# Kernel optimization log

Measured on AMD Instinct MI355X. Metric: run time of the kernel, lower is better.

Reference implementation:

```python
import jax, jax.numpy as jnp
import numpy as np

B, S, H = 2, 2048, 2048
NH, G = 16, 4
HD = H // NH          # 128
REP = NH // G         # 4 query heads per KV group
KV = G * HD           # 512


def setup_inputs() -> dict:
    key = jax.random.key(0)
    ks = jax.random.split(key, 10)
    s = 0.02
    X = jax.random.normal(ks[0], (B, S, H), dtype=jnp.float32)
    Wq = jax.random.normal(ks[1], (H, H), dtype=jnp.float32) * s
    bq = jnp.zeros((H,), dtype=jnp.float32)
    Wk = jax.random.normal(ks[2], (H, KV), dtype=jnp.float32) * s
    bk = jnp.zeros((KV,), dtype=jnp.float32)
    Wv = jax.random.normal(ks[3], (H, KV), dtype=jnp.float32) * s
    bv = jnp.zeros((KV,), dtype=jnp.float32)
    Wo = jax.random.normal(ks[4], (H, H), dtype=jnp.float32) * s
    bo = jnp.zeros((H,), dtype=jnp.float32)
    # causal mask: 1 where attention is disallowed (strict upper triangle)
    casual_mask = jnp.triu(jnp.ones((S, S), dtype=jnp.float32), k=1)[None, None]
    return {"X": X, "Wq": Wq, "bq": bq, "Wk": Wk, "bk": bk,
            "Wv": Wv, "bv": bv, "Wo": Wo, "bo": bo,
            "casual_mask": casual_mask}


def reference(X, Wq, bq, Wk, bk, Wv, bv, Wo, bo, casual_mask):
    # projections
    q = X @ Wq + bq                          # [B,S,H]
    k = X @ Wk + bk                          # [B,S,G*HD]
    v = X @ Wv + bv                          # [B,S,G*HD]
    # split heads; q grouped as (group, rep) to match torch expand ordering
    q = q.reshape(B, S, NH, HD).transpose(0, 2, 1, 3)       # [B,NH,S,HD]
    q = q.reshape(B, G, REP, S, HD)                          # [B,G,REP,S,HD]
    k = k.reshape(B, S, G, HD).transpose(0, 2, 1, 3)         # [B,G,S,HD]
    v = v.reshape(B, S, G, HD).transpose(0, 2, 1, 3)         # [B,G,S,HD]
    scale = 1.0 / jnp.sqrt(jnp.float32(HD))
    scores = jnp.einsum('bgrqd,bgkd->bgrqk', q, k) * scale   # [B,G,REP,S,S]
    scores = scores + casual_mask * (-1e9)
    probs = jax.nn.softmax(scores, axis=-1)
    out = jnp.einsum('bgrqk,bgkd->bgrqd', probs, v)          # [B,G,REP,S,HD]
    out = out.reshape(B, NH, S, HD).transpose(0, 2, 1, 3).reshape(B, S, H)
    return out @ Wo + bo
```

## Files before the change

kernel.cpp:

```cpp
#include <hip/hip_runtime.h>

#define B_   2
#define S_   2048
#define H_   2048
#define NH_  16
#define G_   4
#define HD_  128
#define KV_  512
#define HQKV 3072

typedef __attribute__((ext_vector_type(8))) short bf16x8;
typedef __attribute__((ext_vector_type(4))) float f32x4;

__device__ __forceinline__ unsigned short f2bf(float f) {
    unsigned u = __float_as_uint(f);
    u += 0x7fff + ((u >> 16) & 1);
    return (unsigned short)(u >> 16);
}
__device__ __forceinline__ float bf2f(unsigned short s) {
    return __uint_as_float(((unsigned)s) << 16);
}
__device__ __forceinline__ unsigned cvtpk(float a, float b) {
    unsigned r;
    asm volatile("v_cvt_pk_bf16_f32 %0, %1, %2" : "=v"(r) : "v"(a), "v"(b));
    return r;
}

#define GLDS16(gsrc, ldst)                                                            \
    __builtin_amdgcn_global_load_lds(                                                 \
        (const __attribute__((address_space(1))) void*)(gsrc),                        \
        (__attribute__((address_space(3))) void*)(ldst), 16, 0, 0)

#define SC2F (0.08838834764831843f * 1.4426950408889634f)

__global__ void k_cvt_bf16(const float* __restrict__ in, unsigned short* __restrict__ out, int n4) {
    int i = blockIdx.x * blockDim.x + threadIdx.x;
    if (i >= n4) return;
    float4 v = ((const float4*)in)[i];
    ushort4 o;
    o.x = f2bf(v.x); o.y = f2bf(v.y); o.z = f2bf(v.z); o.w = f2bf(v.w);
    ((ushort4*)out)[i] = o;
}

__global__ void k_transpose_cvt(const float* __restrict__ in, unsigned short* __restrict__ out,
                                int R, int C) {
    __shared__ float t[32][33];
    int c0 = blockIdx.x * 32, r0 = blockIdx.y * 32;
    int tx = threadIdx.x, ty = threadIdx.y;
#pragma unroll
    for (int i = 0; i < 4; ++i)
        t[ty + i*8][tx] = in[(size_t)(r0 + ty + i*8) * C + c0 + tx];
    __syncthreads();
#pragma unroll
    for (int i = 0; i < 4; ++i)
        out[(size_t)(c0 + ty + i*8) * R + r0 + tx] = f2bf(t[tx][ty + i*8]);
}

__global__ void k_transpose_qkv(const float* __restrict__ Wq, const float* __restrict__ Wk,
                                const float* __restrict__ Wv, unsigned short* __restrict__ out) {
    __shared__ float t[32][33];
    int n0g = blockIdx.x * 32;
    int h0 = blockIdx.y * 32;
    const float* src; int C, n0l;
    if (n0g < H_)            { src = Wq; C = H_;  n0l = n0g; }
    else if (n0g < H_ + KV_) { src = Wk; C = KV_; n0l = n0g - H_; }
    else                     { src = Wv; C = KV_; n0l = n0g - H_ - KV_; }
    int tx = threadIdx.x, ty = threadIdx.y;
#pragma unroll
    for (int i = 0; i < 4; ++i)
        t[ty + i*8][tx] = src[(size_t)(h0 + ty + i*8) * C + n0l + tx];
    __syncthreads();
#pragma unroll
    for (int i = 0; i < 4; ++i)
        out[(size_t)(n0g + ty + i*8) * H_ + h0 + tx] = f2bf(t[tx][ty + i*8]);
}

__global__ void k_concat_bias(const float* __restrict__ bq, const float* __restrict__ bk,
                              const float* __restrict__ bv, float* __restrict__ out) {
    int i = blockIdx.x * 256 + threadIdx.x;
    if (i >= HQKV) return;
    out[i] = (i < H_) ? bq[i] : (i < H_ + KV_ ? bk[i - H_] : bv[i - H_ - KV_]);
}

__global__ void k_transpose_v(const unsigned short* __restrict__ in, unsigned short* __restrict__ out) {
    __shared__ unsigned short t[32][33];
    int b = blockIdx.z;
    int c0 = blockIdx.x * 32, s0 = blockIdx.y * 32;
    int tx = threadIdx.x, ty = threadIdx.y;
#pragma unroll
    for (int i = 0; i < 4; ++i)
        t[ty + i*8][tx] = in[((size_t)b * S_ + s0 + ty + i*8) * HQKV + (H_ + KV_) + c0 + tx];
    __syncthreads();
#pragma unroll
    for (int i = 0; i < 4; ++i)
        out[((size_t)b * KV_ + c0 + ty + i*8) * S_ + s0 + tx] = t[tx][ty + i*8];
}

template <bool BF16OUT, bool QSCALE>
__global__ __launch_bounds__(512, 2) void k_gemm256(
    const unsigned short* __restrict__ A, const unsigned short* __restrict__ Bt,
    const float* __restrict__ bias, void* __restrict__ Cout, int M, int N, int K) {
    __shared__ __align__(16) unsigned short As[2][256 * 64];
    __shared__ __align__(16) unsigned short Bs[2][256 * 64];
    const int tid = threadIdx.x, lane = tid & 63;
    const int w = tid >> 6;
    const int l15 = lane & 15, l4 = lane >> 4;
    const int wr = w >> 2, wc = w & 3;
    const int m0 = blockIdx.x * 256, n0 = blockIdx.y * 256;
    f32x4 acc[8][4] = {};

    auto stageA = [&](int buf, int kt, int h) {
#pragma unroll
        for (int i = 0; i < 2; ++i) {
            int p = i * 512 + tid;
            int j = p >> 3;
            int row = h * 64 + (j >> 6) * 128 + (j & 63);
            int sc = p & 7;
            int c = sc ^ (row & 7);
            GLDS16(A + (size_t)(m0 + row) * K + kt * 64 + c * 8,
                   &As[buf][(row * 8 + sc) * 8]);
        }
    };
    auto stageB = [&](int buf, int kt, int h) {
#pragma unroll
        for (int i = 0; i < 2; ++i) {
            int p = i * 512 + tid;
            int j = p >> 3;
            int row = h * 32 + (j >> 5) * 64 + (j & 31);
            int sc = p & 7;
            int c = sc ^ (row & 7);
            GLDS16(Bt + (size_t)(n0 + row) * K + kt * 64 + c * 8,
                   &Bs[buf][(row * 8 + sc) * 8]);
        }
    };

    const int NT = K >> 6;
    stageB(0, 0, 0); stageA(0, 0, 0); stageB(0, 0, 1); stageA(0, 0, 1);
    stageB(1, 1, 0); stageA(1, 1, 0);

    bf16x8 bf[2][2];
    for (int t = 0; t < NT; ++t) {
        const int cur = t & 1, nxt = cur ^ 1;
        if (t == NT - 1) { asm volatile("s_waitcnt vmcnt(0)" ::: "memory"); }
        else             { asm volatile("s_waitcnt vmcnt(4)" ::: "memory"); }
        __builtin_amdgcn_s_barrier();
        __builtin_amdgcn_sched_barrier(0);

#pragma unroll
        for (int q = 0; q < 4; ++q) {
            const int nh = q >> 1, mh = q & 1;
            bf16x8 af[4][2];
#pragma unroll
            for (int mf2 = 0; mf2 < 4; ++mf2)
#pragma unroll
                for (int ks = 0; ks < 2; ++ks) {
                    int row = wr * 128 + (mh * 4 + mf2) * 16 + l15;
                    int ch = (ks * 4 + l4) ^ (row & 7);
                    af[mf2][ks] = *(const bf16x8*)(&As[cur][(row * 8 + ch) * 8]);
                }
            if (mh == 0) {
#pragma unroll
                for (int nf2 = 0; nf2 < 2; ++nf2)
#pragma unroll
                    for (int ks = 0; ks < 2; ++ks) {
                        int row = wc * 64 + (nh * 2 + nf2) * 16 + l15;
                        int ch = (ks * 4 + l4) ^ (row & 7);
                        bf[nf2][ks] = *(const bf16x8*)(&Bs[cur][(row * 8 + ch) * 8]);
                    }
            }
            if (q == 0)      { if (t + 1 < NT) stageB(nxt, t + 1, 1); }
            else if (q == 1) { if (t + 1 < NT) stageA(nxt, t + 1, 1); }
            else if (q == 2) { if (t + 2 < NT) stageB(cur, t + 2, 0); }
            else             { if (t + 2 < NT) stageA(cur, t + 2, 0); }

            __builtin_amdgcn_sched_barrier(0);
            __builtin_amdgcn_s_barrier();
            asm volatile("s_waitcnt lgkmcnt(0)" ::: "memory");
            __builtin_amdgcn_sched_barrier(0);
            __builtin_amdgcn_s_setprio(1);
#pragma unroll
            for (int mf2 = 0; mf2 < 4; ++mf2)
#pragma unroll
                for (int nf2 = 0; nf2 < 2; ++nf2)
#pragma unroll
                    for (int ks = 0; ks < 2; ++ks)
                        acc[mh * 4 + mf2][nh * 2 + nf2] = __builtin_amdgcn_mfma_f32_16x16x32_bf16(
                            af[mf2][ks], bf[nf2][ks], acc[mh * 4 + mf2][nh * 2 + nf2], 0, 0, 0);
            __builtin_amdgcn_s_setprio(0);
            __builtin_amdgcn_s_barrier();
        }
    }

#pragma unroll
    for (int mf = 0; mf < 8; ++mf) {
        int row = m0 + wr * 128 + mf * 16 + l4 * 4;
#pragma unroll
        for (int nf = 0; nf < 4; ++nf) {
            int col = n0 + wc * 64 + nf * 16 + l15;
            float bv = bias[col];
#pragma unroll
            for (int r = 0; r < 4; ++r) {
                float v = acc[mf][nf][r] + bv;
                if (QSCALE) { if (col < H_) v *= SC2F; }
                if (BF16OUT)
                    ((unsigned short*)Cout)[(size_t)(row + r) * N + col] = f2bf(v);
                else
                    ((float*)Cout)[(size_t)(row + r) * N + col] = v;
            }
        }
    }
}

template <bool BF16OUT, bool QSCALE>
__global__ __launch_bounds__(256) void k_gemm_bt(
    const unsigned short* __restrict__ A, const unsigned short* __restrict__ Bt,
    const float* __restrict__ bias, void* __restrict__ Cout, int M, int N, int K) {
    __shared__ __align__(16) unsigned short As[128 * 64];
    __shared__ __align__(16) unsigned short Bs[128 * 64];
    const int tid = threadIdx.x, lane = tid & 63, w = tid >> 6;
    const int l15 = lane & 15, l4 = lane >> 4;
    const int wr = w >> 1, wc = w & 1;
    const int m0 = blockIdx.x * 128, n0 = blockIdx.y * 128;
    f32x4 acc[4][4] = {};

    for (int kt = 0; kt < K; kt += 64) {
        __syncthreads();
#pragma unroll
        for (int i = 0; i < 4; ++i) {
            int p = (w * 4 + i) * 64 + lane;
            int row = p >> 3, c = (p & 7) ^ (row & 7);
            GLDS16(A + (size_t)(m0 + row) * K + kt + c * 8, As + (size_t)(w * 4 + i) * 512);
        }
#pragma unroll
        for (int i = 0; i < 4; ++i) {
            int p = (w * 4 + i) * 64 + lane;
            int row = p >> 3, c = (p & 7) ^ (row & 7);
            GLDS16(Bt + (size_t)(n0 + row) * K + kt + c * 8, Bs + (size_t)(w * 4 + i) * 512);
        }
        __syncthreads();
#pragma unroll
        for (int ks = 0; ks < 2; ++ks) {
            bf16x8 af[4], bfr[4];
#pragma unroll
            for (int m = 0; m < 4; ++m) {
                int row = wr * 64 + m * 16 + l15;
                int ch = (ks * 4 + l4) ^ (row & 7);
                af[m] = *(const bf16x8*)(As + row * 64 + ch * 8);
            }
#pragma unroll
            for (int n = 0; n < 4; ++n) {
                int row = wc * 64 + n * 16 + l15;
                int ch = (ks * 4 + l4) ^ (row & 7);
                bfr[n] = *(const bf16x8*)(Bs + row * 64 + ch * 8);
            }
#pragma unroll
            for (int m = 0; m < 4; ++m)
#pragma unroll
                for (int n = 0; n < 4; ++n)
                    acc[m][n] = __builtin_amdgcn_mfma_f32_16x16x32_bf16(af[m], bfr[n], acc[m][n], 0, 0, 0);
        }
    }
#pragma unroll
    for (int m = 0; m < 4; ++m) {
        int row = m0 + wr * 64 + m * 16 + l4 * 4;
#pragma unroll
        for (int n = 0; n < 4; ++n) {
            int col = n0 + wc * 64 + n * 16 + l15;
            float bv = bias[col];
#pragma unroll
            for (int r = 0; r < 4; ++r) {
                float v = acc[m][n][r] + bv;
                if (QSCALE) { if (col < H_) v *= SC2F; }
                if (BF16OUT)
                    ((unsigned short*)Cout)[(size_t)(row + r) * N + col] = f2bf(v);
                else
                    ((float*)Cout)[(size_t)(row + r) * N + col] = v;
            }
        }
    }
}

__global__ __launch_bounds__(256, 4) void k_flash(
    const unsigned short* __restrict__ QKV,
    const unsigned short* __restrict__ VT,
    unsigned short* __restrict__ Oa,
    unsigned short* __restrict__ part1,
    float* __restrict__ mlbuf) {
    __shared__ __align__(16) unsigned short Ks[64 * 128];
    __shared__ __align__(16) unsigned short Vs[128 * 64];
    const int tid = threadIdx.x, lane = tid & 63, w = tid >> 6;
    const int l15 = lane & 15, l4 = lane >> 4;
    const int bid = blockIdx.x;
    const int xcd = bid & 7, idx = bid >> 3;
    const int bh = xcd * 4 + (idx & 3);
    const int jidx = idx >> 2;
    const int b = bh >> 4, nh = bh & 15, g = nh >> 2;

    int qt, t0, t1, mode;
    if (jidx < 16) { qt = 16 + jidx; t0 = 0; t1 = 16; mode = 1; }
    else {
        int k = jidx - 16, j = k >> 1;
        if ((k & 1) == 0) { qt = 31 - j; t0 = 16; t1 = qt + 1; mode = 2; }
        else              { qt = 15 - j; t0 = 0;  t1 = qt + 1; mode = 0; }
    }
    const int qbase = qt * 64 + w * 16;

    const unsigned short* kgbase = QKV + (size_t)b * S_ * HQKV + H_ + g * HD_;
    const unsigned short* vgbase = VT + ((size_t)b * KV_ + g * HD_) * S_;

    auto issueK = [&](int kt) {
        const int kv0 = kt * 64;
#pragma unroll
        for (int i = 0; i < 4; ++i) {
            int p = i * 256 + tid;
            int row = p >> 4, c = (p & 15) ^ (row & 15);
            GLDS16(kgbase + (size_t)(kv0 + row) * HQKV + c * 8, &Ks[(i * 256 + w * 64) * 8]);
        }
    };
    auto issueV = [&](int kt) {
        const int kv0 = kt * 64;
#pragma unroll
        for (int i = 0; i < 4; ++i) {
            int p = i * 256 + tid;
            int row = p >> 3, c = (p & 7) ^ (row & 7);
            GLDS16(vgbase + (size_t)row * S_ + kv0 + c * 8, &Vs[(i * 256 + w * 64) * 8]);
        }
    };

    bf16x8 qf[4];
#pragma unroll
    for (int kb = 0; kb < 4; ++kb)
        qf[kb] = *(const bf16x8*)(QKV + (size_t)(b * S_ + qbase + l15) * HQKV +
                                  nh * HD_ + kb * 32 + l4 * 8);

    f32x4 o[8] = {};
    float m_r = -1e30f, l_r = 0.f;

    const int src0 = l15 + 16 * ((2 * l4) & 3);
    const int src1 = l15 + 16 * ((2 * l4 + 1) & 3);
    const bool hsel = ((l4 >> 1) & 1) != 0;

    issueK(t0);
    issueV(t0);

    for (int kt = t0; kt < t1; ++kt) {
        const int kv0 = kt * 64;
        asm volatile("s_waitcnt vmcnt(4)" ::: "memory");
        __builtin_amdgcn_s_barrier();
        __builtin_amdgcn_sched_barrier(0);

        f32x4 s[4] = {};
#pragma unroll
        for (int kb = 0; kb < 4; ++kb) {
            bf16x8 kf[4];
#pragma unroll
            for (int n = 0; n < 4; ++n) {
                int row = n * 16 + l15;
                int sl = (kb * 4 + l4) ^ (row & 15);
                kf[n] = *(const bf16x8*)(&Ks[(row * 16 + sl) * 8]);
            }
            __builtin_amdgcn_s_setprio(1);
#pragma unroll
            for (int n = 0; n < 4; ++n)
                s[n] = __builtin_amdgcn_mfma_f32_16x16x32_bf16(kf[n], qf[kb], s[n], 0, 0, 0);
            __builtin_amdgcn_s_setprio(0);
        }
        if (kv0 + 63 > qbase) {
            const int qrow = qbase + l15;
#pragma unroll
            for (int n = 0; n < 4; ++n)
#pragma unroll
                for (int r = 0; r < 4; ++r) {
                    int kcol = kv0 + n * 16 + l4 * 4 + r;
                    if (kcol > qrow) s[n][r] = -1e30f;
                }
        }
        float pmax = s[0][0];
#pragma unroll
        for (int n = 0; n < 4; ++n)
#pragma unroll
            for (int r = 0; r < 4; ++r) pmax = fmaxf(pmax, s[n][r]);
        pmax = fmaxf(pmax, __shfl_xor(pmax, 16));
        pmax = fmaxf(pmax, __shfl_xor(pmax, 32));
        if (__any(pmax > m_r + 8.0f)) {
            float mn = fmaxf(m_r, pmax);
            float sf = exp2f(m_r - mn);
            m_r = mn;
            l_r *= sf;
#pragma unroll
            for (int nc = 0; nc < 8; ++nc) {
                f32x4 t = o[nc];
                t[0] *= sf; t[1] *= sf; t[2] *= sf; t[3] *= sf;
                o[nc] = t;
            }
        }
        float rsum = 0.f;
#pragma unroll
        for (int n = 0; n < 4; ++n)
#pragma unroll
            for (int r = 0; r < 4; ++r) {
                float p = exp2f(s[n][r] - m_r);
                s[n][r] = p;
                rsum += p;
            }
        rsum += __shfl_xor(rsum, 16);
        rsum += __shfl_xor(rsum, 32);
        l_r += rsum;

        unsigned plo[4], phi[4];
#pragma unroll
        for (int n = 0; n < 4; ++n) {
            plo[n] = cvtpk(s[n][0], s[n][1]);
            phi[n] = cvtpk(s[n][2], s[n][3]);
        }

        asm volatile("s_waitcnt vmcnt(0)" ::: "memory");
        __builtin_amdgcn_s_barrier();
        __builtin_amdgcn_sched_barrier(0);
        if (kt + 1 < t1) issueK(kt + 1);

#pragma unroll
        for (int kb = 0; kb < 2; ++kb) {
            const int n0i = 2 * kb, n1i = 2 * kb + 1;
            unsigned a0, a1, w0, w1, w2, w3;
            a0 = __shfl((int)plo[n0i], src0); a1 = __shfl((int)plo[n1i], src0); w0 = hsel ? a1 : a0;
            a0 = __shfl((int)phi[n0i], src0); a1 = __shfl((int)phi[n1i], src0); w1 = hsel ? a1 : a0;
            a0 = __shfl((int)plo[n0i], src1); a1 = __shfl((int)plo[n1i], src1); w2 = hsel ? a1 : a0;
            a0 = __shfl((int)phi[n0i], src1); a1 = __shfl((int)phi[n1i], src1); w3 = hsel ? a1 : a0;
            int4 pw = make_int4((int)w0, (int)w1, (int)w2, (int)w3);
            bf16x8 pf = *(bf16x8*)&pw;
            __builtin_amdgcn_s_setprio(1);
#pragma unroll
            for (int nc = 0; nc < 8; ++nc) {
                int row = nc * 16 + l15;
                int sl = (kb * 4 + l4) ^ (row & 7);
                bf16x8 vf = *(const bf16x8*)(&Vs[(row * 8 + sl) * 8]);
                o[nc] = __builtin_amdgcn_mfma_f32_16x16x32_bf16(vf, pf, o[nc], 0, 0, 0);
            }
            __builtin_amdgcn_s_setprio(0);
        }

        __builtin_amdgcn_s_barrier();
        __builtin_amdgcn_sched_barrier(0);
        if (kt + 1 < t1) issueV(kt + 1);
    }

    const int qrow = qbase + l15;
    if (mode == 0) {
        float inv = 1.0f / l_r;
        size_t base = (size_t)(b * S_ + qrow) * H_ + nh * HD_ + l4 * 4;
#pragma unroll
        for (int nc = 0; nc < 8; ++nc) {
            uint2 pk;
            pk.x = cvtpk(o[nc][0] * inv, o[nc][1] * inv);
            pk.y = cvtpk(o[nc][2] * inv, o[nc][3] * inv);
            *(uint2*)(Oa + base + nc * 16) = pk;
        }
    } else {
        const int base = bh * 16 + (qt - 16);
        const int c = (mode == 1) ? 0 : 1;
        float* mlrec = mlbuf + (size_t)(base * 2 + c) * 64 * 2;
        if (l4 == 0) {
            int row = w * 16 + l15;
            mlrec[row * 2 + 0] = m_r;
            mlrec[row * 2 + 1] = l_r;
        }
        if (mode == 1) {
            size_t ob = (size_t)(b * S_ + qrow) * H_ + nh * HD_ + l4 * 4;
#pragma unroll
            for (int nc = 0; nc < 8; ++nc) {
                uint2 pk;
                pk.x = cvtpk(o[nc][0], o[nc][1]);
                pk.y = cvtpk(o[nc][2], o[nc][3]);
                *(uint2*)(Oa + ob + nc * 16) = pk;
            }
        } else {
            size_t pb = ((size_t)base * 64 + w * 16 + l15) * 128 + l4 * 4;
#pragma unroll
            for (int nc = 0; nc < 8; ++nc) {
                uint2 pk;
                pk.x = cvtpk(o[nc][0], o[nc][1]);
                pk.y = cvtpk(o[nc][2], o[nc][3]);
                *(uint2*)(part1 + pb + nc * 16) = pk;
            }
        }
    }
}

__global__ __launch_bounds__(256) void k_combine(
    const float* __restrict__ mlbuf, const unsigned short* __restrict__ part1,
    unsigned short* __restrict__ Oa) {
    int rec = blockIdx.x;
    int bh = rec >> 4, qt = 16 + (rec & 15);
    int b = bh >> 4, nh = bh & 15;
    int row = threadIdx.x >> 2;
    int dseg = (threadIdx.x & 3) * 32;
    const float* ml0 = mlbuf + (size_t)(rec * 2 + 0) * 128;
    const float* ml1 = mlbuf + (size_t)(rec * 2 + 1) * 128;
    float m0 = ml0[row * 2], l0 = ml0[row * 2 + 1];
    float m1 = ml1[row * 2], l1 = ml1[row * 2 + 1];
    float M = fmaxf(m0, m1);
    float a0 = exp2f(m0 - M), a1 = exp2f(m1 - M);
    float L = a0 * l0 + a1 * l1;
    float s0 = a0 / L, s1 = a1 / L;
    size_t ob = ((size_t)(b * S_) + qt * 64 + row) * H_ + nh * HD_ + dseg;
    const unsigned short* p1 = part1 + ((size_t)rec * 64 + row) * 128 + dseg;
#pragma unroll
    for (int i = 0; i < 4; ++i) {
        bf16x8 v0 = *(const bf16x8*)(Oa + ob + i * 8);
        bf16x8 v1 = *(const bf16x8*)(p1 + i * 8);
        bf16x8 oo;
#pragma unroll
        for (int e = 0; e < 8; ++e)
            oo[e] = (short)f2bf(bf2f((unsigned short)v0[e]) * s0 +
                                bf2f((unsigned short)v1[e]) * s1);
        *(bf16x8*)(Oa + ob + i * 8) = oo;
    }
}

extern "C" void kernel_launch(void* const* d_in, const int* in_sizes, int n_in,
                              void* d_out, int out_size, void* d_ws, size_t ws_size,
                              hipStream_t stream) {
    const float* X  = (const float*)d_in[0];
    const float* Wq = (const float*)d_in[1];
    const float* bq = (const float*)d_in[2];
    const float* Wk = (const float*)d_in[3];
    const float* bk = (const float*)d_in[4];
    const float* Wv = (const float*)d_in[5];
    const float* bv = (const float*)d_in[6];
    const float* Wo = (const float*)d_in[7];
    const float* bo = (const float*)d_in[8];
    float* out = (float*)d_out;

    if (ws_size < 80000000) return;
    char* ws = (char*)d_ws;
    unsigned short* Xb    = (unsigned short*)(ws);
    unsigned short* WqkvT = (unsigned short*)(ws + 16777216);
    unsigned short* WoT   = (unsigned short*)(ws + 29360128);
    unsigned short* QKV   = (unsigned short*)(ws + 37748736);
    unsigned short* VbT   = (unsigned short*)(ws + 62914560);
    unsigned short* part1 = (unsigned short*)(ws + 67108864);
    float*          mlbuf = (float*)(ws + 75497472);
    float*          bqkv  = (float*)(ws + 76021760);
    unsigned short* AOb   = Xb;

    k_cvt_bf16<<<(B_ * S_ * H_ / 4 + 255) / 256, 256, 0, stream>>>(X, Xb, B_ * S_ * H_ / 4);
    k_transpose_qkv<<<dim3(HQKV / 32, H_ / 32), dim3(32, 8), 0, stream>>>(Wq, Wk, Wv, WqkvT);
    k_transpose_cvt<<<dim3(H_ / 32, H_ / 32), dim3(32, 8), 0, stream>>>(Wo, WoT, H_, H_);
    k_concat_bias<<<(HQKV + 255) / 256, 256, 0, stream>>>(bq, bk, bv, bqkv);

    k_gemm256<true, true><<<dim3(16, 12), 512, 0, stream>>>(Xb, WqkvT, bqkv, QKV, 4096, HQKV, 2048);

    k_transpose_v<<<dim3(KV_ / 32, S_ / 32, B_), dim3(32, 8), 0, stream>>>(QKV, VbT);
    k_flash<<<dim3(1536), 256, 0, stream>>>(QKV, VbT, AOb, part1, mlbuf);
    k_combine<<<dim3(512), 256, 0, stream>>>(mlbuf, part1, AOb);

    k_gemm_bt<false, false><<<dim3(32, 16), 256, 0, stream>>>(AOb, WoT, bo, out, 4096, 2048, 2048);
}
```

Measured before the change: 208.2 us.

## Double Q tile per wave in flash attention and double-buffer output GEMM

Each flash-attention wave now handles two 16-row query groups (128 rows per block), so every K/V fragment read from LDS feeds twice as many MFMAs. The grid is halved and the split/combine bookkeeping is rescaled to match. Occupancy drops from 4 to 3 blocks because each wave holds more registers. The output projection GEMM gains a two-stage LDS double buffer, so the next tile's global-to-LDS loads overlap with the current tile's compute.

```diff
diff --git a/kernel.cpp b/kernel.cpp
--- a/kernel.cpp
+++ b/kernel.cpp
@@ -212,64 +212,82 @@
 }
 
 template <bool BF16OUT, bool QSCALE>
-__global__ __launch_bounds__(256) void k_gemm_bt(
+__global__ __launch_bounds__(256) void k_gemm128p(
     const unsigned short* __restrict__ A, const unsigned short* __restrict__ Bt,
     const float* __restrict__ bias, void* __restrict__ Cout, int M, int N, int K) {
-    __shared__ __align__(16) unsigned short As[128 * 64];
-    __shared__ __align__(16) unsigned short Bs[128 * 64];
+    __shared__ __align__(16) unsigned short As[2][128 * 64];
+    __shared__ __align__(16) unsigned short Bs[2][128 * 64];
     const int tid = threadIdx.x, lane = tid & 63, w = tid >> 6;
     const int l15 = lane & 15, l4 = lane >> 4;
     const int wr = w >> 1, wc = w & 1;
     const int m0 = blockIdx.x * 128, n0 = blockIdx.y * 128;
     f32x4 acc[4][4] = {};
 
-    for (int kt = 0; kt < K; kt += 64) {
-        __syncthreads();
+    auto stage = [&](int buf, int kt) {
 #pragma unroll
         for (int i = 0; i < 4; ++i) {
             int p = (w * 4 + i) * 64 + lane;
             int row = p >> 3, c = (p & 7) ^ (row & 7);
-            GLDS16(A + (size_t)(m0 + row) * K + kt + c * 8, As + (size_t)(w * 4 + i) * 512);
+            GLDS16(A + (size_t)(m0 + row) * K + kt * 64 + c * 8, &As[buf][(w * 4 + i) * 512]);
         }
 #pragma unroll
         for (int i = 0; i < 4; ++i) {
             int p = (w * 4 + i) * 64 + lane;
             int row = p >> 3, c = (p & 7) ^ (row & 7);
-            GLDS16(Bt + (size_t)(n0 + row) * K + kt + c * 8, Bs + (size_t)(w * 4 + i) * 512);
-        }
-        __syncthreads();
-#pragma unroll
-        for (int ks = 0; ks < 2; ++ks) {
-            bf16x8 af[4], bfr[4];
-#pragma unroll
-            for (int m = 0; m < 4; ++m) {
-                int row = wr * 64 + m * 16 + l15;
-                int ch = (ks * 4 + l4) ^ (row & 7);
-                af[m] = *(const bf16x8*)(As + row * 64 + ch * 8);
-            }
+            GLDS16(Bt + (size_t)(n0 + row) * K + kt * 64 + c * 8, &Bs[buf][(w * 4 + i) * 512]);
+        }
+    };
+
+    const int NT = K >> 6;
+    stage(0, 0);
+    if (NT > 1) stage(1, 1);
+
+    for (int t = 0; t < NT; ++t) {
+        const int cur = t & 1;
+        if (t + 1 < NT) { asm volatile("s_waitcnt vmcnt(8)" ::: "memory"); }
+        else            { asm volatile("s_waitcnt vmcnt(0)" ::: "memory"); }
+        __builtin_amdgcn_s_barrier();
+        __builtin_amdgcn_sched_barrier(0);
+
+        bf16x8 bfr[2][4];
+#pragma unroll
+        for (int ks = 0; ks < 2; ++ks)
 #pragma unroll
             for (int n = 0; n < 4; ++n) {
                 int row = wc * 64 + n * 16 + l15;
-                int ch = (ks * 4 + l4) ^ (row & 7);
-                bfr[n] = *(const bf16x8*)(Bs + row * 64 + ch * 8);
-            }
-#pragma unroll
-            for (int m = 0; m < 4; ++m)
-#pragma unroll
-                for (int n = 0; n < 4; ++n)
-                    acc[m][n] = __builtin_amdgcn_mfma_f32_16x16x32_bf16(af[m], bfr[n], acc[m][n], 0, 0, 0);
-        }
-    }
-#pragma unroll
-    for (int m = 0; m < 4; ++m) {
-        int row = m0 + wr * 64 + m * 16 + l4 * 4;
+                int sl = (ks * 4 + l4) ^ (row & 7);
+                bfr[ks][n] = *(const bf16x8*)(&Bs[cur][(row * 8 + sl) * 8]);
+            }
+#pragma unroll
+        for (int fr = 0; fr < 4; ++fr) {
+            int row = wr * 64 + fr * 16 + l15;
+            bf16x8 af0 = *(const bf16x8*)(&As[cur][(row * 8 + (l4 ^ (row & 7))) * 8]);
+            bf16x8 af1 = *(const bf16x8*)(&As[cur][(row * 8 + ((4 + l4) ^ (row & 7))) * 8]);
+            __builtin_amdgcn_s_setprio(1);
+#pragma unroll
+            for (int n = 0; n < 4; ++n)
+                acc[fr][n] = __builtin_amdgcn_mfma_f32_16x16x32_bf16(af0, bfr[0][n], acc[fr][n], 0, 0, 0);
+#pragma unroll
+            for (int n = 0; n < 4; ++n)
+                acc[fr][n] = __builtin_amdgcn_mfma_f32_16x16x32_bf16(af1, bfr[1][n], acc[fr][n], 0, 0, 0);
+            __builtin_amdgcn_s_setprio(0);
+        }
+
+        __builtin_amdgcn_s_barrier();
+        __builtin_amdgcn_sched_barrier(0);
+        if (t + 2 < NT) stage(cur, t + 2);
+    }
+
+#pragma unroll
+    for (int fr = 0; fr < 4; ++fr) {
+        int row = m0 + wr * 64 + fr * 16 + l4 * 4;
 #pragma unroll
         for (int n = 0; n < 4; ++n) {
             int col = n0 + wc * 64 + n * 16 + l15;
             float bv = bias[col];
 #pragma unroll
             for (int r = 0; r < 4; ++r) {
-                float v = acc[m][n][r] + bv;
+                float v = acc[fr][n][r] + bv;
                 if (QSCALE) { if (col < H_) v *= SC2F; }
                 if (BF16OUT)
                     ((unsigned short*)Cout)[(size_t)(row + r) * N + col] = f2bf(v);
@@ -280,7 +298,7 @@
     }
 }
 
-__global__ __launch_bounds__(256, 4) void k_flash(
+__global__ __launch_bounds__(256, 3) void k_flash(
     const unsigned short* __restrict__ QKV,
     const unsigned short* __restrict__ VT,
     unsigned short* __restrict__ Oa,
@@ -297,13 +315,13 @@
     const int b = bh >> 4, nh = bh & 15, g = nh >> 2;
 
     int qt, t0, t1, mode;
-    if (jidx < 16) { qt = 16 + jidx; t0 = 0; t1 = 16; mode = 1; }
+    if (jidx < 8) { qt = 8 + jidx; t0 = 0; t1 = 16; mode = 1; }
     else {
-        int k = jidx - 16, j = k >> 1;
-        if ((k & 1) == 0) { qt = 31 - j; t0 = 16; t1 = qt + 1; mode = 2; }
-        else              { qt = 15 - j; t0 = 0;  t1 = qt + 1; mode = 0; }
-    }
-    const int qbase = qt * 64 + w * 16;
+        int k = jidx - 8, j = k >> 1;
+        if ((k & 1) == 0) { qt = 15 - j; t0 = 16; t1 = 2 * qt + 2; mode = 2; }
+        else              { qt = 7 - j;  t0 = 0;  t1 = 2 * qt + 2; mode = 0; }
+    }
+    const int qbase = qt * 128 + w * 32;
 
     const unsigned short* kgbase = QKV + (size_t)b * S_ * HQKV + H_ + g * HD_;
     const unsigned short* vgbase = VT + ((size_t)b * KV_ + g * HD_) * S_;
@@ -327,14 +345,16 @@
         }
     };
 
-    bf16x8 qf[4];
-#pragma unroll
-    for (int kb = 0; kb < 4; ++kb)
-        qf[kb] = *(const bf16x8*)(QKV + (size_t)(b * S_ + qbase + l15) * HQKV +
-                                  nh * HD_ + kb * 32 + l4 * 8);
-
-    f32x4 o[8] = {};
-    float m_r = -1e30f, l_r = 0.f;
+    bf16x8 qf[2][4];
+#pragma unroll
+    for (int g2 = 0; g2 < 2; ++g2)
+#pragma unroll
+        for (int kb = 0; kb < 4; ++kb)
+            qf[g2][kb] = *(const bf16x8*)(QKV + (size_t)(b * S_ + qbase + g2 * 16 + l15) * HQKV +
+                                          nh * HD_ + kb * 32 + l4 * 8);
+
+    f32x4 o[2][8] = {};
+    float m_r[2] = {-1e30f, -1e30f}, l_r[2] = {0.f, 0.f};
 
     const int src0 = l15 + 16 * ((2 * l4) & 3);
     const int src1 = l15 + 16 * ((2 * l4 + 1) & 3);
@@ -349,7 +369,7 @@
         __builtin_amdgcn_s_barrier();
         __builtin_amdgcn_sched_barrier(0);
 
-        f32x4 s[4] = {};
+        f32x4 s[2][4] = {};
 #pragma unroll
         for (int kb = 0; kb < 4; ++kb) {
             bf16x8 kf[4];
@@ -361,57 +381,64 @@
             }
             __builtin_amdgcn_s_setprio(1);
 #pragma unroll
+            for (int g2 = 0; g2 < 2; ++g2)
+#pragma unroll
+                for (int n = 0; n < 4; ++n)
+                    s[g2][n] = __builtin_amdgcn_mfma_f32_16x16x32_bf16(kf[n], qf[g2][kb], s[g2][n], 0, 0, 0);
+            __builtin_amdgcn_s_setprio(0);
+        }
+        if (kv0 + 63 > qbase) {
+#pragma unroll
+            for (int g2 = 0; g2 < 2; ++g2) {
+                const int qrow = qbase + g2 * 16 + l15;
+#pragma unroll
+                for (int n = 0; n < 4; ++n)
+#pragma unroll
+                    for (int r = 0; r < 4; ++r) {
+                        int kcol = kv0 + n * 16 + l4 * 4 + r;
+                        if (kcol > qrow) s[g2][n][r] = -1e30f;
+                    }
+            }
+        }
+        unsigned plo[2][4], phi[2][4];
+#pragma unroll
+        for (int g2 = 0; g2 < 2; ++g2) {
+            float pmax = s[g2][0][0];
+#pragma unroll
             for (int n = 0; n < 4; ++n)
-                s[n] = __builtin_amdgcn_mfma_f32_16x16x32_bf16(kf[n], qf[kb], s[n], 0, 0, 0);
-            __builtin_amdgcn_s_setprio(0);
-        }
-        if (kv0 + 63 > qbase) {
-            const int qrow = qbase + l15;
+#pragma unroll
+                for (int r = 0; r < 4; ++r) pmax = fmaxf(pmax, s[g2][n][r]);
+            pmax = fmaxf(pmax, __shfl_xor(pmax, 16));
+            pmax = fmaxf(pmax, __shfl_xor(pmax, 32));
+            if (__any(pmax > m_r[g2] + 8.0f)) {
+                float mn = fmaxf(m_r[g2], pmax);
+                float sf = exp2f(m_r[g2] - mn);
+                m_r[g2] = mn;
+                l_r[g2] *= sf;
+#pragma unroll
+                for (int nc = 0; nc < 8; ++nc) {
+                    f32x4 t = o[g2][nc];
+                    t[0] *= sf; t[1] *= sf; t[2] *= sf; t[3] *= sf;
+                    o[g2][nc] = t;
+                }
+            }
+            float rsum = 0.f;
 #pragma unroll
             for (int n = 0; n < 4; ++n)
 #pragma unroll
                 for (int r = 0; r < 4; ++r) {
-                    int kcol = kv0 + n * 16 + l4 * 4 + r;
-                    if (kcol > qrow) s[n][r] = -1e30f;
+                    float p = exp2f(s[g2][n][r] - m_r[g2]);
+                    s[g2][n][r] = p;
+                    rsum += p;
                 }
-        }
-        float pmax = s[0][0];
-#pragma unroll
-        for (int n = 0; n < 4; ++n)
-#pragma unroll
-            for (int r = 0; r < 4; ++r) pmax = fmaxf(pmax, s[n][r]);
-        pmax = fmaxf(pmax, __shfl_xor(pmax, 16));
-        pmax = fmaxf(pmax, __shfl_xor(pmax, 32));
-        if (__any(pmax > m_r + 8.0f)) {
-            float mn = fmaxf(m_r, pmax);
-            float sf = exp2f(m_r - mn);
-            m_r = mn;
-            l_r *= sf;
-#pragma unroll
-            for (int nc = 0; nc < 8; ++nc) {
-                f32x4 t = o[nc];
-                t[0] *= sf; t[1] *= sf; t[2] *= sf; t[3] *= sf;
-                o[nc] = t;
-            }
-        }
-        float rsum = 0.f;
-#pragma unroll
-        for (int n = 0; n < 4; ++n)
-#pragma unroll
-            for (int r = 0; r < 4; ++r) {
-                float p = exp2f(s[n][r] - m_r);
-                s[n][r] = p;
-                rsum += p;
-            }
-        rsum += __shfl_xor(rsum, 16);
-        rsum += __shfl_xor(rsum, 32);
-        l_r += rsum;
-
-        unsigned plo[4], phi[4];
-#pragma unroll
-        for (int n = 0; n < 4; ++n) {
-            plo[n] = cvtpk(s[n][0], s[n][1]);
-            phi[n] = cvtpk(s[n][2], s[n][3]);
+            rsum += __shfl_xor(rsum, 16);
+            rsum += __shfl_xor(rsum, 32);
+            l_r[g2] += rsum;
+#pragma unroll
+            for (int n = 0; n < 4; ++n) {
+                plo[g2][n] = cvtpk(s[g2][n][0], s[g2][n][1]);
+                phi[g2][n] = cvtpk(s[g2][n][2], s[g2][n][3]);
+            }
         }
 
         asm volatile("s_waitcnt vmcnt(0)" ::: "memory");
@@ -422,20 +449,25 @@
 #pragma unroll
         for (int kb = 0; kb < 2; ++kb) {
             const int n0i = 2 * kb, n1i = 2 * kb + 1;
-            unsigned a0, a1, w0, w1, w2, w3;
-            a0 = __shfl((int)plo[n0i], src0); a1 = __shfl((int)plo[n1i], src0); w0 = hsel ? a1 : a0;
-            a0 = __shfl((int)phi[n0i], src0); a1 = __shfl((int)phi[n1i], src0); w1 = hsel ? a1 : a0;
-            a0 = __shfl((int)plo[n0i], src1); a1 = __shfl((int)plo[n1i], src1); w2 = hsel ? a1 : a0;
-            a0 = __shfl((int)phi[n0i], src1); a1 = __shfl((int)phi[n1i], src1); w3 = hsel ? a1 : a0;
-            int4 pw = make_int4((int)w0, (int)w1, (int)w2, (int)w3);
-            bf16x8 pf = *(bf16x8*)&pw;
+            bf16x8 pf[2];
+#pragma unroll
+            for (int g2 = 0; g2 < 2; ++g2) {
+                unsigned a0, a1, w0, w1, w2, w3;
+                a0 = __shfl((int)plo[g2][n0i], src0); a1 = __shfl((int)plo[g2][n1i], src0); w0 = hsel ? a1 : a0;
+                a0 = __shfl((int)phi[g2][n0i], src0); a1 = __shfl((int)phi[g2][n1i], src0); w1 = hsel ? a1 : a0;
+                a0 = __shfl((int)plo[g2][n0i], src1); a1 = __shfl((int)plo[g2][n1i], src1); w2 = hsel ? a1 : a0;
+                a0 = __shfl((int)phi[g2][n0i], src1); a1 = __shfl((int)phi[g2][n1i], src1); w3 = hsel ? a1 : a0;
+                int4 pw = make_int4((int)w0, (int)w1, (int)w2, (int)w3);
+                pf[g2] = *(bf16x8*)&pw;
+            }
             __builtin_amdgcn_s_setprio(1);
 #pragma unroll
             for (int nc = 0; nc < 8; ++nc) {
                 int row = nc * 16 + l15;
                 int sl = (kb * 4 + l4) ^ (row & 7);
                 bf16x8 vf = *(const bf16x8*)(&Vs[(row * 8 + sl) * 8]);
-                o[nc] = __builtin_amdgcn_mfma_f32_16x16x32_bf16(vf, pf, o[nc], 0, 0, 0);
+                o[0][nc] = __builtin_amdgcn_mfma_f32_16x16x32_bf16(vf, pf[0], o[0][nc], 0, 0, 0);
+                o[1][nc] = __builtin_amdgcn_mfma_f32_16x16x32_bf16(vf, pf[1], o[1][nc], 0, 0, 0);
             }
             __builtin_amdgcn_s_setprio(0);
         }
@@ -445,43 +477,56 @@
         if (kt + 1 < t1) issueV(kt + 1);
     }
 
-    const int qrow = qbase + l15;
     if (mode == 0) {
-        float inv = 1.0f / l_r;
-        size_t base = (size_t)(b * S_ + qrow) * H_ + nh * HD_ + l4 * 4;
-#pragma unroll
-        for (int nc = 0; nc < 8; ++nc) {
-            uint2 pk;
-            pk.x = cvtpk(o[nc][0] * inv, o[nc][1] * inv);
-            pk.y = cvtpk(o[nc][2] * inv, o[nc][3] * inv);
-            *(uint2*)(Oa + base + nc * 16) = pk;
-        }
-    } else {
-        const int base = bh * 16 + (qt - 16);
-        const int c = (mode == 1) ? 0 : 1;
-        float* mlrec = mlbuf + (size_t)(base * 2 + c) * 64 * 2;
-        if (l4 == 0) {
-            int row = w * 16 + l15;
-            mlrec[row * 2 + 0] = m_r;
-            mlrec[row * 2 + 1] = l_r;
-        }
-        if (mode == 1) {
-            size_t ob = (size_t)(b * S_ + qrow) * H_ + nh * HD_ + l4 * 4;
+#pragma unroll
+        for (int g2 = 0; g2 < 2; ++g2) {
+            float inv = 1.0f / l_r[g2];
+            int qrow = qbase + g2 * 16 + l15;
+            size_t base = (size_t)(b * S_ + qrow) * H_ + nh * HD_ + l4 * 4;
 #pragma unroll
             for (int nc = 0; nc < 8; ++nc) {
                 uint2 pk;
-                pk.x = cvtpk(o[nc][0], o[nc][1]);
-                pk.y = cvtpk(o[nc][2], o[nc][3]);
-                *(uint2*)(Oa + ob + nc * 16) = pk;
+                pk.x = cvtpk(o[g2][nc][0] * inv, o[g2][nc][1] * inv);
+                pk.y = cvtpk(o[g2][nc][2] * inv, o[g2][nc][3] * inv);
+                *(uint2*)(Oa + base + nc * 16) = pk;
+            }
+        }
+    } else {
+        const int base = bh * 8 + (qt - 8);
+        const int c = (mode == 1) ? 0 : 1;
+        float* mlrec = mlbuf + (size_t)(base * 2 + c) * 256;
+        if (l4 == 0) {
+#pragma unroll
+            for (int g2 = 0; g2 < 2; ++g2) {
+                int row = w * 32 + g2 * 16 + l15;
+                mlrec[row * 2 + 0] = m_r[g2];
+                mlrec[row * 2 + 1] = l_r[g2];
+            }
+        }
+        if (mode == 1) {
+#pragma unroll
+            for (int g2 = 0; g2 < 2; ++g2) {
+                int qrow = qbase + g2 * 16 + l15;
+                size_t ob = (size_t)(b * S_ + qrow) * H_ + nh * HD_ + l4 * 4;
+#pragma unroll
+                for (int nc = 0; nc < 8; ++nc) {
+                    uint2 pk;
+                    pk.x = cvtpk(o[g2][nc][0], o[g2][nc][1]);
+                    pk.y = cvtpk(o[g2][nc][2], o[g2][nc][3]);
+                    *(uint2*)(Oa + ob + nc * 16) = pk;
+                }
             }
         } else {
-            size_t pb = ((size_t)base * 64 + w * 16 + l15) * 128 + l4 * 4;
-#pragma unroll
-            for (int nc = 0; nc < 8; ++nc) {
-                uint2 pk;
-                pk.x = cvtpk(o[nc][0], o[nc][1]);
-                pk.y = cvtpk(o[nc][2], o[nc][3]);
-                *(uint2*)(part1 + pb + nc * 16) = pk;
+#pragma unroll
+            for (int g2 = 0; g2 < 2; ++g2) {
+                size_t pb = ((size_t)base * 128 + w * 32 + g2 * 16 + l15) * 128 + l4 * 4;
+#pragma unroll
+                for (int nc = 0; nc < 8; ++nc) {
+                    uint2 pk;
+                    pk.x = cvtpk(o[g2][nc][0], o[g2][nc][1]);
+                    pk.y = cvtpk(o[g2][nc][2], o[g2][nc][3]);
+                    *(uint2*)(part1 + pb + nc * 16) = pk;
+                }
             }
         }
     }
@@ -491,22 +536,22 @@
     const float* __restrict__ mlbuf, const unsigned short* __restrict__ part1,
     unsigned short* __restrict__ Oa) {
     int rec = blockIdx.x;
-    int bh = rec >> 4, qt = 16 + (rec & 15);
+    int bh = rec >> 3, qt = 8 + (rec & 7);
     int b = bh >> 4, nh = bh & 15;
-    int row = threadIdx.x >> 2;
-    int dseg = (threadIdx.x & 3) * 32;
-    const float* ml0 = mlbuf + (size_t)(rec * 2 + 0) * 128;
-    const float* ml1 = mlbuf + (size_t)(rec * 2 + 1) * 128;
+    int row = threadIdx.x >> 1;
+    int dseg = (threadIdx.x & 1) * 64;
+    const float* ml0 = mlbuf + (size_t)(rec * 2 + 0) * 256;
+    const float* ml1 = mlbuf + (size_t)(rec * 2 + 1) * 256;
     float m0 = ml0[row * 2], l0 = ml0[row * 2 + 1];
     float m1 = ml1[row * 2], l1 = ml1[row * 2 + 1];
     float M = fmaxf(m0, m1);
     float a0 = exp2f(m0 - M), a1 = exp2f(m1 - M);
     float L = a0 * l0 + a1 * l1;
     float s0 = a0 / L, s1 = a1 / L;
-    size_t ob = ((size_t)(b * S_) + qt * 64 + row) * H_ + nh * HD_ + dseg;
-    const unsigned short* p1 = part1 + ((size_t)rec * 64 + row) * 128 + dseg;
-#pragma unroll
-    for (int i = 0; i < 4; ++i) {
+    size_t ob = ((size_t)(b * S_) + qt * 128 + row) * H_ + nh * HD_ + dseg;
+    const unsigned short* p1 = part1 + ((size_t)rec * 128 + row) * 128 + dseg;
+#pragma unroll
+    for (int i = 0; i < 8; ++i) {
         bf16x8 v0 = *(const bf16x8*)(Oa + ob + i * 8);
         bf16x8 v1 = *(const bf16x8*)(p1 + i * 8);
         bf16x8 oo;
@@ -552,8 +597,8 @@
     k_gemm256<true, true><<<dim3(16, 12), 512, 0, stream>>>(Xb, WqkvT, bqkv, QKV, 4096, HQKV, 2048);
 
     k_transpose_v<<<dim3(KV_ / 32, S_ / 32, B_), dim3(32, 8), 0, stream>>>(QKV, VbT);
-    k_flash<<<dim3(1536), 256, 0, stream>>>(QKV, VbT, AOb, part1, mlbuf);
-    k_combine<<<dim3(512), 256, 0, stream>>>(mlbuf, part1, AOb);
-
-    k_gemm_bt<false, false><<<dim3(32, 16), 256, 0, stream>>>(AOb, WoT, bo, out, 4096, 2048, 2048);
-}
+    k_flash<<<dim3(768), 256, 0, stream>>>(QKV, VbT, AOb, part1, mlbuf);
+    k_combine<<<dim3(256), 256, 0, stream>>>(mlbuf, part1, AOb);
+
+    k_gemm128p<false, false><<<dim3(32, 16), 256, 0, stream>>>(AOb, WoT, bo, out, 4096, 2048, 2048);
+}
```

Measured after the change: 232.6 us. 11.7% more time.

## Replace output-projection GEMM with double-buffered 256x128 pipelined kernel

Applied to the files above, without the earlier changes.

Replaces the simple 128x128 single-buffered output-projection GEMM with a 256x128 tile kernel using 8 waves, double-buffered LDS, and interleaved global-to-LDS prefetch of the next two K tiles across compute quarters. Explicit waitcnt, sched barriers and setprio are used to overlap loads with MFMA work. The grid drops from 512 to 256 blocks, which may underfill the 256 CUs and trades occupancy for per-block efficiency.

```diff
diff --git a/kernel.cpp b/kernel.cpp
--- a/kernel.cpp
+++ b/kernel.cpp
@@ -211,66 +211,103 @@
     }
 }
 
-template <bool BF16OUT, bool QSCALE>
-__global__ __launch_bounds__(256) void k_gemm_bt(
+template <bool BF16OUT>
+__global__ __launch_bounds__(512, 1) void k_gemm256x128(
     const unsigned short* __restrict__ A, const unsigned short* __restrict__ Bt,
     const float* __restrict__ bias, void* __restrict__ Cout, int M, int N, int K) {
-    __shared__ __align__(16) unsigned short As[128 * 64];
-    __shared__ __align__(16) unsigned short Bs[128 * 64];
-    const int tid = threadIdx.x, lane = tid & 63, w = tid >> 6;
+    __shared__ __align__(16) unsigned short As[2][256 * 64];
+    __shared__ __align__(16) unsigned short Bs[2][128 * 64];
+    const int tid = threadIdx.x, lane = tid & 63;
+    const int w = tid >> 6;
     const int l15 = lane & 15, l4 = lane >> 4;
-    const int wr = w >> 1, wc = w & 1;
-    const int m0 = blockIdx.x * 128, n0 = blockIdx.y * 128;
-    f32x4 acc[4][4] = {};
-
-    for (int kt = 0; kt < K; kt += 64) {
-        __syncthreads();
-#pragma unroll
-        for (int i = 0; i < 4; ++i) {
-            int p = (w * 4 + i) * 64 + lane;
-            int row = p >> 3, c = (p & 7) ^ (row & 7);
-            GLDS16(A + (size_t)(m0 + row) * K + kt + c * 8, As + (size_t)(w * 4 + i) * 512);
-        }
-#pragma unroll
-        for (int i = 0; i < 4; ++i) {
-            int p = (w * 4 + i) * 64 + lane;
-            int row = p >> 3, c = (p & 7) ^ (row & 7);
-            GLDS16(Bt + (size_t)(n0 + row) * K + kt + c * 8, Bs + (size_t)(w * 4 + i) * 512);
-        }
-        __syncthreads();
-#pragma unroll
-        for (int ks = 0; ks < 2; ++ks) {
-            bf16x8 af[4], bfr[4];
-#pragma unroll
-            for (int m = 0; m < 4; ++m) {
-                int row = wr * 64 + m * 16 + l15;
-                int ch = (ks * 4 + l4) ^ (row & 7);
-                af[m] = *(const bf16x8*)(As + row * 64 + ch * 8);
-            }
-#pragma unroll
-            for (int n = 0; n < 4; ++n) {
-                int row = wc * 64 + n * 16 + l15;
-                int ch = (ks * 4 + l4) ^ (row & 7);
-                bfr[n] = *(const bf16x8*)(Bs + row * 64 + ch * 8);
-            }
-#pragma unroll
-            for (int m = 0; m < 4; ++m)
-#pragma unroll
-                for (int n = 0; n < 4; ++n)
-                    acc[m][n] = __builtin_amdgcn_mfma_f32_16x16x32_bf16(af[m], bfr[n], acc[m][n], 0, 0, 0);
-        }
-    }
-#pragma unroll
-    for (int m = 0; m < 4; ++m) {
-        int row = m0 + wr * 64 + m * 16 + l4 * 4;
-#pragma unroll
-        for (int n = 0; n < 4; ++n) {
-            int col = n0 + wc * 64 + n * 16 + l15;
+    const int wr = w >> 2, wc = w & 3;
+    const int m0 = blockIdx.x * 256, n0 = blockIdx.y * 128;
+    f32x4 acc[8][2] = {};
+
+    auto stageA = [&](int buf, int kt, int h) {
+#pragma unroll
+        for (int i = 0; i < 2; ++i) {
+            int p = i * 512 + tid;
+            int j = p >> 3;
+            int row = h * 64 + (j >> 6) * 128 + (j & 63);
+            int sc = p & 7;
+            int c = sc ^ (row & 7);
+            GLDS16(A + (size_t)(m0 + row) * K + kt * 64 + c * 8,
+                   &As[buf][(row * 8 + sc) * 8]);
+        }
+    };
+    auto stageB = [&](int buf, int kt, int h) {
+        int j = tid >> 3;
+        int row = h * 16 + (j >> 4) * 32 + (j & 15);
+        int sc = tid & 7;
+        int c = sc ^ (row & 7);
+        GLDS16(Bt + (size_t)(n0 + row) * K + kt * 64 + c * 8,
+               &Bs[buf][(row * 8 + sc) * 8]);
+    };
+
+    const int NT = K >> 6;
+    stageB(0, 0, 0); stageA(0, 0, 0); stageB(0, 0, 1); stageA(0, 0, 1);
+    stageB(1, 1, 0); stageA(1, 1, 0);
+
+    bf16x8 bf[2];
+    for (int t = 0; t < NT; ++t) {
+        const int cur = t & 1, nxt = cur ^ 1;
+        if (t == NT - 1) { asm volatile("s_waitcnt vmcnt(0)" ::: "memory"); }
+        else             { asm volatile("s_waitcnt vmcnt(3)" ::: "memory"); }
+        __builtin_amdgcn_s_barrier();
+        __builtin_amdgcn_sched_barrier(0);
+
+#pragma unroll
+        for (int q = 0; q < 4; ++q) {
+            const int nh = q >> 1, mh = q & 1;
+            bf16x8 af[4][2];
+#pragma unroll
+            for (int mf2 = 0; mf2 < 4; ++mf2)
+#pragma unroll
+                for (int ks = 0; ks < 2; ++ks) {
+                    int row = wr * 128 + (mh * 4 + mf2) * 16 + l15;
+                    int ch = (ks * 4 + l4) ^ (row & 7);
+                    af[mf2][ks] = *(const bf16x8*)(&As[cur][(row * 8 + ch) * 8]);
+                }
+            if (mh == 0) {
+#pragma unroll
+                for (int ks = 0; ks < 2; ++ks) {
+                    int row = wc * 32 + nh * 16 + l15;
+                    int ch = (ks * 4 + l4) ^ (row & 7);
+                    bf[ks] = *(const bf16x8*)(&Bs[cur][(row * 8 + ch) * 8]);
+                }
+            }
+            if (q == 0)      { if (t + 1 < NT) stageB(nxt, t + 1, 1); }
+            else if (q == 1) { if (t + 1 < NT) stageA(nxt, t + 1, 1); }
+            else if (q == 2) { if (t + 2 < NT) stageB(cur, t + 2, 0); }
+            else             { if (t + 2 < NT) stageA(cur, t + 2, 0); }
+
+            __builtin_amdgcn_sched_barrier(0);
+            __builtin_amdgcn_s_barrier();
+            asm volatile("s_waitcnt lgkmcnt(0)" ::: "memory");
+            __builtin_amdgcn_sched_barrier(0);
+            __builtin_amdgcn_s_setprio(1);
+#pragma unroll
+            for (int mf2 = 0; mf2 < 4; ++mf2)
+#pragma unroll
+                for (int ks = 0; ks < 2; ++ks)
+                    acc[mh * 4 + mf2][nh] = __builtin_amdgcn_mfma_f32_16x16x32_bf16(
+                        af[mf2][ks], bf[ks], acc[mh * 4 + mf2][nh], 0, 0, 0);
+            __builtin_amdgcn_s_setprio(0);
+            __builtin_amdgcn_s_barrier();
+        }
+    }
+
+#pragma unroll
+    for (int mf = 0; mf < 8; ++mf) {
+        int row = m0 + wr * 128 + mf * 16 + l4 * 4;
+#pragma unroll
+        for (int nf = 0; nf < 2; ++nf) {
+            int col = n0 + wc * 32 + nf * 16 + l15;
             float bv = bias[col];
 #pragma unroll
             for (int r = 0; r < 4; ++r) {
-                float v = acc[m][n][r] + bv;
-                if (QSCALE) { if (col < H_) v *= SC2F; }
+                float v = acc[mf][nf][r] + bv;
                 if (BF16OUT)
                     ((unsigned short*)Cout)[(size_t)(row + r) * N + col] = f2bf(v);
                 else
@@ -555,5 +592,5 @@
     k_flash<<<dim3(1536), 256, 0, stream>>>(QKV, VbT, AOb, part1, mlbuf);
     k_combine<<<dim3(512), 256, 0, stream>>>(mlbuf, part1, AOb);
 
-    k_gemm_bt<false, false><<<dim3(32, 16), 256, 0, stream>>>(AOb, WoT, bo, out, 4096, 2048, 2048);
-}
+    k_gemm256x128<false><<<dim3(16, 16), 512, 0, stream>>>(AOb, WoT, bo, out, 4096, 2048, 2048);
+}
```

After: 217.0 us. 4.2% more time.
